# Optimization experiments

Measured on AMD Instinct MI355X. Metric: run time of the kernel, lower is better.

Reference implementation:

```python
import jax, jax.numpy as jnp
import numpy as np

PATCH = 3
PAD = 1  # (patchsize-1)//2
PRETRAIN_DIM = 1024
TARGET_DIM = 1024
OUT_H, OUT_W = 224, 224


def _pool_matrix(L_in, L_out):
    """Matrix P s.t. x @ P == torch.adaptive_avg_pool1d(x, L_out)."""
    P = np.zeros((L_in, L_out), dtype=np.float32)
    for i in range(L_out):
        s = (i * L_in) // L_out
        e = -((-(i + 1) * L_in) // L_out)  # ceil
        P[s:e, i] = 1.0 / (e - s)
    return jnp.asarray(P)


def patchify(x):
    """[B,C,H,W] -> [B,H*W,C,3,3], matching Unfold(k=3,s=1,p=1) + reshape/permute."""
    B, C, H, W = x.shape
    xp = jnp.pad(x, ((0, 0), (0, 0), (PAD, PAD), (PAD, PAD)))
    # [B,C,3,3,H,W] with kernel offsets (ki,kj)
    cols = jnp.stack([
        jnp.stack([xp[:, :, i:i + H, j:j + W] for j in range(PATCH)], axis=3)
        for i in range(PATCH)], axis=2)
    return cols.transpose(0, 4, 5, 1, 2, 3).reshape(B, H * W, C, PATCH, PATCH)


def resize_bilinear(x, oh, ow):
    """Bilinear resize of last two dims, align_corners=False (torch semantics)."""
    H, W = x.shape[-2], x.shape[-1]

    def idx(L, O):
        src = (jnp.arange(O, dtype=jnp.float32) + 0.5) * (L / O) - 0.5
        src = jnp.clip(src, 0.0, L - 1)
        i0 = jnp.floor(src).astype(jnp.int32)
        i1 = jnp.minimum(i0 + 1, L - 1)
        return i0, i1, src - i0

    r0, r1, wr = idx(H, oh)
    c0, c1, wc = idx(W, ow)
    xr = x[..., r0, :] * (1.0 - wr)[:, None] + x[..., r1, :] * wr[:, None]
    return xr[..., c0] * (1.0 - wc) + xr[..., c1] * wc


def setup_inputs() -> dict:
    key = jax.random.key(0)
    k1, k2, k3 = jax.random.split(key, 3)
    return {
        "feat1": jax.random.normal(k1, (8, 512, 28, 28), dtype=jnp.float32),
        "feat2": jax.random.normal(k2, (8, 1024, 14, 14), dtype=jnp.float32),
        "memory": jax.random.normal(k3, (20000, 1024), dtype=jnp.float32),
    }


def reference(feat1, feat2, memory):
    B, C1, H1, W1 = feat1.shape
    _, C2, H2, W2 = feat2.shape
    N = H1 * W1  # reference patch grid

    # --- patchify (Unfold k=3 s=1 p=1) ---
    p1 = patchify(feat1)                      # [B, N, C1, 3, 3]
    p2 = patchify(feat2)                      # [B, H2*W2, C2, 3, 3]

    # --- multiscale bilinear resize of layer-2 patch grid to ref grid ---
    g = p2.reshape(B, H2, W2, C2, PATCH, PATCH).transpose(0, 3, 4, 5, 1, 2)  # [B,C2,3,3,H2,W2]
    g = resize_bilinear(g, H1, W1)                                           # [B,C2,3,3,H1,W1]
    p2 = g.transpose(0, 4, 5, 1, 2, 3).reshape(B, N, C2, PATCH, PATCH)

    # --- Preprocessing: adaptive_avg_pool1d over flattened patch -> pretrain dim ---
    f1 = p1.reshape(B * N, C1 * PATCH * PATCH) @ _pool_matrix(C1 * PATCH * PATCH, PRETRAIN_DIM)
    f2 = p2.reshape(B * N, C2 * PATCH * PATCH) @ _pool_matrix(C2 * PATCH * PATCH, PRETRAIN_DIM)

    # --- Aggregator: stack layers, adaptive pool to target dim ---
    stacked = jnp.stack([f1, f2], axis=1).reshape(B * N, 2 * PRETRAIN_DIM)
    feats = stacked @ _pool_matrix(2 * PRETRAIN_DIM, TARGET_DIM)  # [B*N, D]

    # --- kNN memory-bank scoring (k=1): min Euclidean distance ---
    d2 = (jnp.sum(feats * feats, axis=-1, keepdims=True)
          - 2.0 * feats @ memory.T
          + jnp.sum(memory * memory, axis=-1))  # [B*N, M]
    dist = jnp.sqrt(jnp.maximum(d2, 0.0))
    patch_scores = jnp.min(dist, axis=1)       # [B*N]

    # --- unpatch + score + raw segmentation map ---
    ps = patch_scores.reshape(B, N)
    image_scores = jnp.max(ps, axis=1)                           # [B]
    raw_maps = resize_bilinear(ps.reshape(B, H1, W1), OUT_H, OUT_W)  # [B,224,224]
    return image_scores, raw_maps
```

## Files before the change

### kernel.cpp

```cpp
#include <hip/hip_runtime.h>
#include <hip/hip_bf16.h>
#include <math.h>

#define BQ 8
#define C1N 512
#define N1 784
#define C2N 1024
#define M2 196
#define NROWS 6272
#define MEMN 20000
#define MEMNP 20096
#define DIMK 1024
#define NKB 16
#define SLBB 8192
#define OUTHW 50176
#define NTILEA 49
#define NTILEB 157
#define NWG (NTILEB * NTILEA)

typedef unsigned char u8;
typedef long long i64v;
typedef __attribute__((ext_vector_type(4))) float f32x4;

static __device__ __forceinline__ unsigned int f2ord(float f) {
  unsigned int b = __float_as_uint(f);
  return (b & 0x80000000u) ? ~b : (b | 0x80000000u);
}
static __device__ __forceinline__ float ord2f(unsigned int u) {
  unsigned int b = (u & 0x80000000u) ? (u ^ 0x80000000u) : ~u;
  return __uint_as_float(b);
}

static __device__ __forceinline__ int pack4_fp8(float a, float b, float c, float d) {
  int lo = __builtin_amdgcn_cvt_pk_fp8_f32(a, b, 0, false);
  return __builtin_amdgcn_cvt_pk_fp8_f32(c, d, lo, true);
}
static __device__ __forceinline__ float sumsq4_fp8(int w) {
  float f0 = __builtin_amdgcn_cvt_f32_fp8(w, 0);
  float f1 = __builtin_amdgcn_cvt_f32_fp8(w, 1);
  float f2 = __builtin_amdgcn_cvt_f32_fp8(w, 2);
  float f3 = __builtin_amdgcn_cvt_f32_fp8(w, 3);
  return f0 * f0 + f1 * f1 + f2 * f2 + f3 * f3;
}

static __device__ __forceinline__ void gload16(const void* g, void* l) {
  __builtin_amdgcn_global_load_lds((const __attribute__((address_space(1))) void*)g,
                                   (__attribute__((address_space(3))) void*)l, 16, 0, 0);
}

static __device__ __forceinline__ size_t tiled_idx(int grow, int k) {
  int tile = grow >> 7, row = grow & 127;
  int kb = k >> 6, c = (k >> 3) & 7, e = k & 7;
  return (((size_t)(tile * NKB + kb) * 8 + c) * 128 + row) * 8 + e;
}

static __device__ __forceinline__ float f1val(const float* __restrict__ x, int b, unsigned L) {
  unsigned h = L % 28u; unsigned t = L / 28u;
  unsigned ki = t % 3u; t /= 3u;
  unsigned c = t % 512u; t /= 512u;
  unsigned w = t % 28u; unsigned kj = t / 28u;
  unsigned y = h + ki - 1u;
  unsigned xx = w + kj - 1u;
  if (y >= 28u || xx >= 28u) return 0.f;
  return x[(((size_t)b * 512u + c) * 28u + y) * 28u + xx];
}
static __device__ __forceinline__ float f2val(const float* __restrict__ x, int b, unsigned L) {
  unsigned h = L % 14u; unsigned t = L / 14u;
  unsigned ki = t % 3u; t /= 3u;
  unsigned c = t % 1024u; t /= 1024u;
  unsigned w = t % 14u; unsigned kj = t / 14u;
  unsigned y = h + ki - 1u;
  unsigned xx = w + kj - 1u;
  if (y >= 14u || xx >= 14u) return 0.f;
  return x[(((size_t)b * 1024u + c) * 14u + y) * 14u + xx];
}

__global__ __launch_bounds__(256) void feat_a_fp8(const float* __restrict__ feat1,
                                                  u8* __restrict__ At) {
  int id = blockIdx.x * 256 + threadIdx.x;
  if (id >= BQ * 64 * N1) return;
  int n = id % N1; int t = id / N1;
  int jc = t % 64; int b = t / 64;
  float v[8];
#pragma unroll
  for (int e = 0; e < 8; ++e) {
    int j = jc * 8 + e;
    unsigned L0 = 9u * (unsigned)(512 * n + j);
    float s = 0.f;
#pragma unroll
    for (int u = 0; u < 9; ++u) s += f1val(feat1, b, L0 + u);
    s += f1val(feat1, b, L0 + 4u);
    v[e] = s * 0.1f;
  }
  int w0 = pack4_fp8(v[0], v[1], v[2], v[3]);
  int w1 = pack4_fp8(v[4], v[5], v[6], v[7]);
  *(int2*)&At[tiled_idx(b * N1 + n, jc * 8)] = make_int2(w0, w1);
}

__global__ __launch_bounds__(256) void feat_b_stage1(const float* __restrict__ feat2,
                                                     float* __restrict__ H2all) {
  int b = blockIdx.x / M2;
  int n2 = blockIdx.x % M2;
  for (int i = threadIdx.x; i < 512; i += 256) {
    unsigned L0 = 18u * (unsigned)(512 * n2 + i);
    float s = 0.f;
#pragma unroll
    for (int u = 0; u < 18; ++u) s += f2val(feat2, b, L0 + u);
    H2all[((size_t)b * M2 + n2) * 512 + i] = s * (1.0f / 18.0f);
  }
}

__global__ __launch_bounds__(256) void feat_b_stage2_fp8(const float* __restrict__ H2all,
                                                         u8* __restrict__ At) {
  int id = blockIdx.x * 256 + threadIdx.x;
  if (id >= BQ * 64 * N1) return;
  int n = id % N1; int t = id / N1;
  int ic = t % 64; int b = t / 64;
  int y = n / 28, x = n % 28;
  float sy = 0.5f * (float)y - 0.25f;
  sy = fminf(fmaxf(sy, 0.f), 13.f);
  int y0 = (int)sy, y1 = min(y0 + 1, 13);
  float wy = sy - (float)y0;
  float sx = 0.5f * (float)x - 0.25f;
  sx = fminf(fmaxf(sx, 0.f), 13.f);
  int x0 = (int)sx, x1 = min(x0 + 1, 13);
  float wx = sx - (float)x0;
  float w00 = (1.f - wy) * (1.f - wx), w10 = wy * (1.f - wx);
  float w01 = (1.f - wy) * wx, w11 = wy * wx;
  const float* h00 = H2all + ((size_t)b * M2 + y0 * 14 + x0) * 512 + ic * 8;
  const float* h10 = H2all + ((size_t)b * M2 + y1 * 14 + x0) * 512 + ic * 8;
  const float* h01 = H2all + ((size_t)b * M2 + y0 * 14 + x1) * 512 + ic * 8;
  const float* h11 = H2all + ((size_t)b * M2 + y1 * 14 + x1) * 512 + ic * 8;
  float v[8];
#pragma unroll
  for (int e = 0; e < 8; ++e)
    v[e] = w00 * h00[e] + w10 * h10[e] + w01 * h01[e] + w11 * h11[e];
  int w0 = pack4_fp8(v[0], v[1], v[2], v[3]);
  int w1 = pack4_fp8(v[4], v[5], v[6], v[7]);
  *(int2*)&At[tiled_idx(b * N1 + n, 512 + ic * 8)] = make_int2(w0, w1);
}

__global__ __launch_bounds__(256) void memconv_fp8(const float* __restrict__ mem,
                                                   u8* __restrict__ Bt) {
  int gid = blockIdx.x * 256 + threadIdx.x;
  if (gid >= NTILEB * NKB * 1024) return;
  int tile = gid >> 14;
  int within = gid & 16383;
  int kb = within >> 10;
  int u = within & 1023;
  int c = u >> 7, row = u & 127;
  int n = tile * 128 + row;
  int k0 = kb * 64 + c * 8;
  int w0 = 0, w1 = 0;
  if (n < MEMN) {
    const float* src = mem + (size_t)n * DIMK + k0;
    float4 a = *(const float4*)src;
    float4 b = *(const float4*)(src + 4);
    w0 = pack4_fp8(a.x, a.y, a.z, a.w);
    w1 = pack4_fp8(b.x, b.y, b.z, b.w);
  }
  *(int2*)&Bt[(size_t)gid * 8] = make_int2(w0, w1);
}

__global__ __launch_bounds__(256) void mnorm_fp8(const float* __restrict__ memory,
                                                 float* __restrict__ mnorm) {
  __shared__ float red[4];
  const int row = blockIdx.x;
  const float4 v = *(const float4*)&memory[(size_t)row * DIMK + threadIdx.x * 4];
  int p0 = __builtin_amdgcn_cvt_pk_fp8_f32(v.x, v.y, 0, false);
  float s = sumsq4_fp8(__builtin_amdgcn_cvt_pk_fp8_f32(v.z, v.w, p0, true));
#pragma unroll
  for (int off = 32; off; off >>= 1) s += __shfl_down(s, off, 64);
  if ((threadIdx.x & 63) == 0) red[threadIdx.x >> 6] = s;
  __syncthreads();
  if (threadIdx.x == 0) mnorm[row] = red[0] + red[1] + red[2] + red[3];
}

__global__ __launch_bounds__(256, 3) void dist_min_mfma(const u8* __restrict__ At,
                                                        const u8* __restrict__ Bt,
                                                        const float* __restrict__ mnorm,
                                                        unsigned int* __restrict__ minu) {
  __shared__ __align__(16) u8 LAs[3][SLBB];
  __shared__ __align__(16) u8 LBs[3][SLBB];
  const int t = threadIdx.x;
  const int wave = t >> 6, lane = t & 63;

  int lid = blockIdx.x;
  const int q = NWG / 8, r = NWG % 8;
  int xcd = lid & 7, pos = lid >> 3;
  int wgid = (xcd < r ? xcd * (q + 1) : r * (q + 1) + (xcd - r) * q) + pos;
  int g = wgid / (NTILEB * 7), rem = wgid % (NTILEB * 7);
  int bx = rem / 7;
  int by = g * 7 + rem % 7;
  const int row0 = by * 128, col0 = bx * 128;

  f32x4 acc[4][4];
#pragma unroll
  for (int i = 0; i < 4; ++i)
#pragma unroll
    for (int j = 0; j < 4; ++j) acc[i][j] = (f32x4){0.f, 0.f, 0.f, 0.f};

  const int wr = (wave >> 1) * 64, wc = (wave & 1) * 64;
  const int frow = lane & 15, fc = lane >> 4;
  const int aoff = fc * 1024 + (wr + frow) * 8;
  const int boff = fc * 1024 + (wc + frow) * 8;
  const int soff = wave * 1024 + lane * 16;

  const u8* aG = At + (size_t)by * (NKB * SLBB) + soff;
  const u8* bG = Bt + (size_t)bx * (NKB * SLBB) + soff;

#define STAGE(buf)                                  \
  do {                                              \
    gload16(aG,        &LAs[buf][wave * 1024]);     \
    gload16(aG + 4096, &LAs[buf][4096 + wave * 1024]); \
    gload16(bG,        &LBs[buf][wave * 1024]);     \
    gload16(bG + 4096, &LBs[buf][4096 + wave * 1024]); \
    aG += SLBB; bG += SLBB;                         \
  } while (0)

#define COMPUTE(buf)                                                                         \
  do {                                                                                       \
    _Pragma("unroll") for (int kk = 0; kk < 2; ++kk) {                                       \
      i64v a[4], b[4];                                                                       \
      _Pragma("unroll") for (int mi = 0; mi < 4; ++mi)                                       \
          a[mi] = *(const i64v*)&LAs[buf][kk * 4096 + aoff + mi * 128];                      \
      _Pragma("unroll") for (int ni = 0; ni < 4; ++ni)                                       \
          b[ni] = *(const i64v*)&LBs[buf][kk * 4096 + boff + ni * 128];                      \
      __builtin_amdgcn_s_setprio(1);                                                         \
      _Pragma("unroll") for (int mi = 0; mi < 4; ++mi)                                       \
        _Pragma("unroll") for (int ni = 0; ni < 4; ++ni)                                     \
            acc[mi][ni] = __builtin_amdgcn_mfma_f32_16x16x32_fp8_fp8(a[mi], b[ni],           \
                                                                     acc[mi][ni], 0, 0, 0);  \
      __builtin_amdgcn_s_setprio(0);                                                         \
    }                                                                                        \
  } while (0)

#define WAITBAR(n)                                        \
  do {                                                    \
    asm volatile("s_waitcnt vmcnt(" #n ")" ::: "memory"); \
    __builtin_amdgcn_s_barrier();                         \
  } while (0)

  STAGE(0);
  STAGE(1);
  WAITBAR(4);

#pragma unroll 1
  for (int i = 0; i < 4; ++i) {
    STAGE(2); COMPUTE(0); WAITBAR(4);
    STAGE(0); COMPUTE(1); WAITBAR(4);
    STAGE(1); COMPUTE(2); WAITBAR(4);
  }
  STAGE(2); COMPUTE(0); WAITBAR(4);
  STAGE(0); COMPUTE(1); WAITBAR(4);
  COMPUTE(2); WAITBAR(0);
  COMPUTE(0);
#undef STAGE
#undef COMPUTE
#undef WAITBAR

  float cmn[4];
#pragma unroll
  for (int ni = 0; ni < 4; ++ni) {
    int gn = col0 + wc + ni * 16 + frow;
    cmn[ni] = (gn < MEMN) ? mnorm[gn] : INFINITY;
  }
#pragma unroll
  for (int mi = 0; mi < 4; ++mi) {
#pragma unroll
    for (int rr = 0; rr < 4; ++rr) {
      float v = INFINITY;
#pragma unroll
      for (int ni = 0; ni < 4; ++ni)
        v = fminf(v, fmaf(-2.f, acc[mi][ni][rr], cmn[ni]));
#pragma unroll
      for (int off = 1; off < 16; off <<= 1)
        v = fminf(v, __shfl_xor(v, off, 64));
      if (frow == 0) {
        int grow = row0 + wr + mi * 16 + (lane >> 4) * 4 + rr;
        atomicMin(&minu[grow], f2ord(v));
      }
    }
  }
}


__global__ __launch_bounds__(256) void scores_fused(const u8* __restrict__ At,
                                                    const unsigned int* __restrict__ minu,
                                                    float* __restrict__ scores) {
  int row = blockIdx.x * 4 + (threadIdx.x >> 6);
  int lane = threadIdx.x & 63;
  float s = 0.f;
#pragma unroll
  for (int qq = 0; qq < 2; ++qq) {
    int2 d = *(const int2*)&At[tiled_idx(row, (lane + qq * 64) * 8)];
    s += sumsq4_fp8(d.x);
    s += sumsq4_fp8(d.y);
  }
#pragma unroll
  for (int off = 32; off; off >>= 1) s += __shfl_down(s, off, 64);
  if (lane == 0) scores[row] = sqrtf(fmaxf(s + ord2f(minu[row]), 0.f));
}

__global__ __launch_bounds__(256) void image_max_kernel(const float* __restrict__ scores,
                                                        float* __restrict__ out) {
  __shared__ float red[4];
  const int b = blockIdx.x;
  float m = -INFINITY;
  for (int n = threadIdx.x; n < N1; n += 256) m = fmaxf(m, scores[b * N1 + n]);
#pragma unroll
  for (int off = 32; off; off >>= 1) m = fmaxf(m, __shfl_down(m, off, 64));
  if ((threadIdx.x & 63) == 0) red[threadIdx.x >> 6] = m;
  __syncthreads();
  if (threadIdx.x == 0) out[b] = fmaxf(fmaxf(red[0], red[1]), fmaxf(red[2], red[3]));
}

__global__ __launch_bounds__(256) void upsample_kernel(const float* __restrict__ scores,
                                                       float* __restrict__ out) {
  int o = blockIdx.x * 256 + threadIdx.x;
  if (o >= BQ * OUTHW) return;
  int b = o / OUTHW, rem = o % OUTHW;
  int oy = rem / 224, ox = rem % 224;
  float sy = ((float)oy + 0.5f) * 0.125f - 0.5f;
  sy = fminf(fmaxf(sy, 0.f), 27.f);
  int y0 = (int)sy, y1 = min(y0 + 1, 27);
  float wy = sy - (float)y0;
  float sx = ((float)ox + 0.5f) * 0.125f - 0.5f;
  sx = fminf(fmaxf(sx, 0.f), 27.f);
  int x0 = (int)sx, x1 = min(x0 + 1, 27);
  float wx = sx - (float)x0;
  const float* s = scores + b * N1;
  float v0 = s[y0 * 28 + x0] * (1.f - wy) + s[y1 * 28 + x0] * wy;
  float v1 = s[y0 * 28 + x1] * (1.f - wy) + s[y1 * 28 + x1] * wy;
  out[BQ + o] = v0 * (1.f - wx) + v1 * wx;
}

extern "C" void kernel_launch(void* const* d_in, const int* in_sizes, int n_in,
                              void* d_out, int out_size, void* d_ws, size_t ws_size,
                              hipStream_t stream) {
  const float* feat1 = (const float*)d_in[0];
  const float* feat2 = (const float*)d_in[1];
  const float* memory = (const float*)d_in[2];
  float* out = (float*)d_out;

  char* ws = (char*)d_ws;
  size_t off = 0;
  auto wsalloc = [&](size_t bytes) {
    void* p = ws + off;
    off += (bytes + 255) & ~(size_t)255;
    return p;
  };

  u8* At = (u8*)wsalloc((size_t)NTILEA * NKB * SLBB);
  u8* Bt = (u8*)wsalloc((size_t)NTILEB * NKB * SLBB);
  float* mnorm = (float*)wsalloc((size_t)MEMN * 4);
  unsigned int* minu = (unsigned int*)wsalloc((size_t)NROWS * 4);
  float* scores = (float*)wsalloc((size_t)NROWS * 4);
  float* H2all = (float*)Bt;

  feat_a_fp8<<<(BQ * 64 * N1) / 256, 256, 0, stream>>>(feat1, At);
  feat_b_stage1<<<BQ * M2, 256, 0, stream>>>(feat2, H2all);
  feat_b_stage2_fp8<<<(BQ * 64 * N1) / 256, 256, 0, stream>>>(H2all, At);
  memconv_fp8<<<(NTILEB * NKB * 1024) / 256, 256, 0, stream>>>(memory, Bt);
  mnorm_fp8<<<MEMN, 256, 0, stream>>>(memory, mnorm);
  (void)hipMemsetAsync(minu, 0xFF, (size_t)NROWS * 4, stream);

  dist_min_mfma<<<NWG, 256, 0, stream>>>(At, Bt, mnorm, minu);

  scores_fused<<<NROWS / 4, 256, 0, stream>>>(At, minu, scores);
  image_max_kernel<<<BQ, 256, 0, stream>>>(scores, out);
  upsample_kernel<<<(BQ * OUTHW + 255) / 256, 256, 0, stream>>>(scores, out);
}
```

Before: 363.7 us.

## Load A fragments directly to registers and 4-stage B pipeline in LDS

After: 333.1 us. 8.4% less time.

```diff
diff --git a/kernel.cpp b/kernel.cpp
--- a/kernel.cpp
+++ b/kernel.cpp
@@ -11,15 +11,17 @@
 #define MEMN 20000
 #define MEMNP 20096
 #define DIMK 1024
-#define NKB 16
-#define SLBB 8192
+#define NKB 32
+#define AKB 4096
+#define BKB 4096
 #define OUTHW 50176
 #define NTILEA 49
 #define NTILEB 157
 #define NWG (NTILEB * NTILEA)
 
 typedef unsigned char u8;
-typedef long long i64v;
+typedef long long i64;
+typedef __attribute__((ext_vector_type(2))) long long ll2;
 typedef __attribute__((ext_vector_type(4))) float f32x4;
 
 static __device__ __forceinline__ unsigned int f2ord(float f) {
@@ -48,10 +50,11 @@
                                    (__attribute__((address_space(3))) void*)l, 16, 0, 0);
 }
 
-static __device__ __forceinline__ size_t tiled_idx(int grow, int k) {
+static __device__ __forceinline__ size_t tiled_a_idx(int grow, int k) {
   int tile = grow >> 7, row = grow & 127;
-  int kb = k >> 6, c = (k >> 3) & 7, e = k & 7;
-  return (((size_t)(tile * NKB + kb) * 8 + c) * 128 + row) * 8 + e;
+  int half = row >> 6, mi = (row >> 4) & 3, frow = row & 15;
+  int kb = k >> 5, fc = (k >> 3) & 3, e = k & 7;
+  return ((((((size_t)(tile * NKB + kb) * 2 + half) * 4 + fc) * 16 + frow) * 4 + mi) << 3) + e;
 }
 
 static __device__ __forceinline__ float f1val(const float* __restrict__ x, int b, unsigned L) {
@@ -94,7 +97,7 @@
   }
   int w0 = pack4_fp8(v[0], v[1], v[2], v[3]);
   int w1 = pack4_fp8(v[4], v[5], v[6], v[7]);
-  *(int2*)&At[tiled_idx(b * N1 + n, jc * 8)] = make_int2(w0, w1);
+  *(int2*)&At[tiled_a_idx(b * N1 + n, jc * 8)] = make_int2(w0, w1);
 }
 
 __global__ __launch_bounds__(256) void feat_b_stage1(const float* __restrict__ feat2,
@@ -137,20 +140,20 @@
     v[e] = w00 * h00[e] + w10 * h10[e] + w01 * h01[e] + w11 * h11[e];
   int w0 = pack4_fp8(v[0], v[1], v[2], v[3]);
   int w1 = pack4_fp8(v[4], v[5], v[6], v[7]);
-  *(int2*)&At[tiled_idx(b * N1 + n, 512 + ic * 8)] = make_int2(w0, w1);
+  *(int2*)&At[tiled_a_idx(b * N1 + n, 512 + ic * 8)] = make_int2(w0, w1);
 }
 
 __global__ __launch_bounds__(256) void memconv_fp8(const float* __restrict__ mem,
                                                    u8* __restrict__ Bt) {
   int gid = blockIdx.x * 256 + threadIdx.x;
-  if (gid >= NTILEB * NKB * 1024) return;
+  if (gid >= NTILEB * NKB * 512) return;
   int tile = gid >> 14;
   int within = gid & 16383;
-  int kb = within >> 10;
-  int u = within & 1023;
+  int kb = within >> 9;
+  int u = within & 511;
   int c = u >> 7, row = u & 127;
   int n = tile * 128 + row;
-  int k0 = kb * 64 + c * 8;
+  int k0 = kb * 32 + c * 8;
   int w0 = 0, w1 = 0;
   if (n < MEMN) {
     const float* src = mem + (size_t)n * DIMK + k0;
@@ -176,12 +179,11 @@
   if (threadIdx.x == 0) mnorm[row] = red[0] + red[1] + red[2] + red[3];
 }
 
-__global__ __launch_bounds__(256, 3) void dist_min_mfma(const u8* __restrict__ At,
+__global__ __launch_bounds__(256, 4) void dist_min_mfma(const u8* __restrict__ At,
                                                         const u8* __restrict__ Bt,
                                                         const float* __restrict__ mnorm,
                                                         unsigned int* __restrict__ minu) {
-  __shared__ __align__(16) u8 LAs[3][SLBB];
-  __shared__ __align__(16) u8 LBs[3][SLBB];
+  __shared__ __align__(16) u8 LBs[4][4096];
   const int t = threadIdx.x;
   const int wave = t >> 6, lane = t & 63;
 
@@ -202,62 +204,75 @@
 
   const int wr = (wave >> 1) * 64, wc = (wave & 1) * 64;
   const int frow = lane & 15, fc = lane >> 4;
-  const int aoff = fc * 1024 + (wr + frow) * 8;
+  const int half = wave >> 1;
   const int boff = fc * 1024 + (wc + frow) * 8;
-  const int soff = wave * 1024 + lane * 16;
-
-  const u8* aG = At + (size_t)by * (NKB * SLBB) + soff;
-  const u8* bG = Bt + (size_t)bx * (NKB * SLBB) + soff;
-
-#define STAGE(buf)                                  \
-  do {                                              \
-    gload16(aG,        &LAs[buf][wave * 1024]);     \
-    gload16(aG + 4096, &LAs[buf][4096 + wave * 1024]); \
-    gload16(bG,        &LBs[buf][wave * 1024]);     \
-    gload16(bG + 4096, &LBs[buf][4096 + wave * 1024]); \
-    aG += SLBB; bG += SLBB;                         \
+
+  const u8* aP = At + (size_t)by * (NKB * AKB) + ((half * 4 + fc) * 16 + frow) * 32;
+  const u8* bG = Bt + (size_t)bx * (NKB * BKB) + t * 16;
+
+  ll2 ar0[2], ar1[2];
+
+#define LOAD_A(P, kb)                                        \
+  do {                                                       \
+    const u8* p_ = aP + (size_t)(kb) * AKB;                  \
+    ar##P[0] = *(const ll2*)p_;                              \
+    ar##P[1] = *(const ll2*)(p_ + 16);                       \
   } while (0)
 
-#define COMPUTE(buf)                                                                         \
+#define STAGE_B(S, kb) gload16(bG + (size_t)(kb) * BKB, &LBs[S][wave * 1024])
+
+#define SBAR __builtin_amdgcn_s_barrier()
+#define VMW(n) asm volatile("s_waitcnt vmcnt(" #n ")" ::: "memory")
+
+#define COMPUTE(S, P)                                                                        \
   do {                                                                                       \
-    _Pragma("unroll") for (int kk = 0; kk < 2; ++kk) {                                       \
-      i64v a[4], b[4];                                                                       \
-      _Pragma("unroll") for (int mi = 0; mi < 4; ++mi)                                       \
-          a[mi] = *(const i64v*)&LAs[buf][kk * 4096 + aoff + mi * 128];                      \
-      _Pragma("unroll") for (int ni = 0; ni < 4; ++ni)                                       \
-          b[ni] = *(const i64v*)&LBs[buf][kk * 4096 + boff + ni * 128];                      \
-      __builtin_amdgcn_s_setprio(1);                                                         \
-      _Pragma("unroll") for (int mi = 0; mi < 4; ++mi)                                       \
-        _Pragma("unroll") for (int ni = 0; ni < 4; ++ni)                                     \
-            acc[mi][ni] = __builtin_amdgcn_mfma_f32_16x16x32_fp8_fp8(a[mi], b[ni],           \
-                                                                     acc[mi][ni], 0, 0, 0);  \
-      __builtin_amdgcn_s_setprio(0);                                                         \
+    i64 b[4];                                                                                \
+    _Pragma("unroll") for (int ni = 0; ni < 4; ++ni)                                         \
+        b[ni] = *(const i64*)&LBs[S][boff + ni * 128];                                       \
+    i64 a0_ = ar##P[0].x, a1_ = ar##P[0].y, a2_ = ar##P[1].x, a3_ = ar##P[1].y;              \
+    __builtin_amdgcn_s_setprio(1);                                                           \
+    _Pragma("unroll") for (int ni = 0; ni < 4; ++ni) {                                       \
+      acc[0][ni] = __builtin_amdgcn_mfma_f32_16x16x32_fp8_fp8(a0_, b[ni], acc[0][ni], 0, 0, 0); \
+      acc[1][ni] = __builtin_amdgcn_mfma_f32_16x16x32_fp8_fp8(a1_, b[ni], acc[1][ni], 0, 0, 0); \
+      acc[2][ni] = __builtin_amdgcn_mfma_f32_16x16x32_fp8_fp8(a2_, b[ni], acc[2][ni], 0, 0, 0); \
+      acc[3][ni] = __builtin_amdgcn_mfma_f32_16x16x32_fp8_fp8(a3_, b[ni], acc[3][ni], 0, 0, 0); \
     }                                                                                        \
+    __builtin_amdgcn_s_setprio(0);                                                           \
   } while (0)
 
-#define WAITBAR(n)                                        \
-  do {                                                    \
-    asm volatile("s_waitcnt vmcnt(" #n ")" ::: "memory"); \
-    __builtin_amdgcn_s_barrier();                         \
+#define ITER(S, P, PN, kA, kS)       \
+  do {                               \
+    LOAD_A(PN, kA);                  \
+    STAGE_B((S + 3) & 3, kS);        \
+    COMPUTE(S, P);                   \
+    VMW(6);                          \
+    SBAR;                            \
   } while (0)
 
-  STAGE(0);
-  STAGE(1);
-  WAITBAR(4);
+  LOAD_A(0, 0);
+  STAGE_B(0, 0);
+  STAGE_B(1, 1);
+  STAGE_B(2, 2);
+  VMW(0);
+  SBAR;
 
 #pragma unroll 1
-  for (int i = 0; i < 4; ++i) {
-    STAGE(2); COMPUTE(0); WAITBAR(4);
-    STAGE(0); COMPUTE(1); WAITBAR(4);
-    STAGE(1); COMPUTE(2); WAITBAR(4);
-  }
-  STAGE(2); COMPUTE(0); WAITBAR(4);
-  STAGE(0); COMPUTE(1); WAITBAR(4);
-  COMPUTE(2); WAITBAR(0);
-  COMPUTE(0);
-#undef STAGE
+  for (int i = 0; i < 7; ++i) {
+    int k = i * 4;
+    ITER(0, 0, 1, k + 1, k + 3);
+    ITER(1, 1, 0, k + 2, k + 4);
+    ITER(2, 0, 1, k + 3, k + 5);
+    ITER(3, 1, 0, k + 4, k + 6);
+  }
+  LOAD_A(1, 29); STAGE_B(3, 31); COMPUTE(0, 0); VMW(6); SBAR;
+  LOAD_A(0, 30); COMPUTE(1, 1); VMW(5); SBAR;
+  LOAD_A(1, 31); COMPUTE(2, 0); VMW(4); SBAR;
+  COMPUTE(3, 1);
+#undef ITER
 #undef COMPUTE
-#undef WAITBAR
+#undef LOAD_A
+#undef STAGE_B
+#undef VMW
 
   float cmn[4];
 #pragma unroll
@@ -277,7 +292,7 @@
       for (int off = 1; off < 16; off <<= 1)
         v = fminf(v, __shfl_xor(v, off, 64));
       if (frow == 0) {
-        int grow = row0 + wr + mi * 16 + (lane >> 4) * 4 + rr;
+        int grow = row0 + wr + mi * 16 + fc * 4 + rr;
         atomicMin(&minu[grow], f2ord(v));
       }
     }
@@ -293,7 +308,7 @@
   float s = 0.f;
 #pragma unroll
   for (int qq = 0; qq < 2; ++qq) {
-    int2 d = *(const int2*)&At[tiled_idx(row, (lane + qq * 64) * 8)];
+    int2 d = *(const int2*)&At[tiled_a_idx(row, (lane + qq * 64) * 8)];
     s += sumsq4_fp8(d.x);
     s += sumsq4_fp8(d.y);
   }
@@ -351,8 +366,8 @@
     return p;
   };
 
-  u8* At = (u8*)wsalloc((size_t)NTILEA * NKB * SLBB);
-  u8* Bt = (u8*)wsalloc((size_t)NTILEB * NKB * SLBB);
+  u8* At = (u8*)wsalloc((size_t)NTILEA * NKB * AKB);
+  u8* Bt = (u8*)wsalloc((size_t)NTILEB * NKB * BKB);
   float* mnorm = (float*)wsalloc((size_t)MEMN * 4);
   unsigned int* minu = (unsigned int*)wsalloc((size_t)NROWS * 4);
   float* scores = (float*)wsalloc((size_t)NROWS * 4);
@@ -361,7 +376,7 @@
   feat_a_fp8<<<(BQ * 64 * N1) / 256, 256, 0, stream>>>(feat1, At);
   feat_b_stage1<<<BQ * M2, 256, 0, stream>>>(feat2, H2all);
   feat_b_stage2_fp8<<<(BQ * 64 * N1) / 256, 256, 0, stream>>>(H2all, At);
-  memconv_fp8<<<(NTILEB * NKB * 1024) / 256, 256, 0, stream>>>(memory, Bt);
+  memconv_fp8<<<(NTILEB * NKB * 512) / 256, 256, 0, stream>>>(memory, Bt);
   mnorm_fp8<<<MEMN, 256, 0, stream>>>(memory, mnorm);
   (void)hipMemsetAsync(minu, 0xFF, (size_t)NROWS * 4, stream);
 
```
